# Kernel optimization log

Measured on AMD Instinct MI355X. Metric: run time of the kernel, lower is better.

Reference implementation:

```python
import jax, jax.numpy as jnp
import numpy as np

N_NODES = 50000
N_EDGES = 800000
IN_C, HID_C, OUT_C = 128, 128, 64
N_GRAPHS = 64
NEG_SLOPE = 0.2


def setup_inputs() -> dict:
    key = jax.random.key(0)
    ks = jax.random.split(key, 16)
    x = jax.random.normal(ks[0], (N_NODES, IN_C), dtype=jnp.float32)
    edge_index = jax.random.randint(ks[1], (2, N_EDGES), 0, N_NODES, dtype=jnp.int64)
    batch = jnp.sort(jax.random.randint(ks[2], (N_NODES,), 0, N_GRAPHS, dtype=jnp.int64))
    dims = [(IN_C, HID_C), (HID_C, HID_C), (HID_C, OUT_C)]
    inp = {"x": x, "edge_index": edge_index, "batch": batch}
    for l, (din, dout) in enumerate(dims):
        s = 1.0 / np.sqrt(din)
        inp[f"W{l}"] = jax.random.normal(ks[3 + 4 * l], (din, dout), dtype=jnp.float32) * s
        inp[f"as{l}"] = jax.random.normal(ks[4 + 4 * l], (dout,), dtype=jnp.float32) * 0.1
        inp[f"ad{l}"] = jax.random.normal(ks[5 + 4 * l], (dout,), dtype=jnp.float32) * 0.1
        inp[f"b{l}"] = jnp.zeros((dout,), dtype=jnp.float32)
    return inp


def gat_conv(x, src, dst, W, a_src, a_dst, b, n_nodes):
    # h: [N, dout]
    h = x @ W
    alpha_src = h @ a_src  # [N]
    alpha_dst = h @ a_dst  # [N]
    logits = jax.nn.leaky_relu(alpha_src[src] + alpha_dst[dst], NEG_SLOPE)  # [E]
    # segment softmax over incoming edges of each dst node
    m = jax.ops.segment_max(logits, dst, num_segments=n_nodes)
    e = jnp.exp(logits - m[dst])
    denom = jax.ops.segment_sum(e, dst, num_segments=n_nodes)
    alpha = e / denom[dst]  # [E]
    out = jax.ops.segment_sum(alpha[:, None] * h[src], dst, num_segments=n_nodes)
    return out + b


def reference(x, edge_index, batch, W0, as0, ad0, b0, W1, as1, ad1, b1, W2, as2, ad2, b2):
    n = x.shape[0]
    # add self loops (PyG GATConv default)
    loop = jnp.arange(n, dtype=edge_index.dtype)
    src = jnp.concatenate([edge_index[0], loop])
    dst = jnp.concatenate([edge_index[1], loop])
    h = jax.nn.relu(gat_conv(x, src, dst, W0, as0, ad0, b0, n))
    h = jax.nn.relu(gat_conv(h, src, dst, W1, as1, ad1, b1, n))
    h = gat_conv(h, src, dst, W2, as2, ad2, b2, n)
    # global_add_pool
    return jax.ops.segment_sum(h, batch, num_segments=N_GRAPHS)
```

## Files before the change

### kernel.cpp

```cpp
#include <hip/hip_runtime.h>
#include <hip/hip_fp16.h>
#include <math.h>

#define N_NODES 50000
#define N_EDGES 800000
#define N_GRAPHS 64
#define NEG_SLOPE 0.2f
#define SLOTS 64

#define BIN_NODES 256
#define NBINS 196
#define CAP 6144
#define P1_BLOCKS 192
#define BATCH 2048

typedef _Float16 f16x8 __attribute__((ext_vector_type(8)));
typedef float f32x4 __attribute__((ext_vector_type(4)));

__device__ __forceinline__ float leaky(float x) {
    return x > 0.f ? x : NEG_SLOPE * x;
}

struct __align__(8) half4 {
    __half2 a, b;
};

__global__ __launch_bounds__(256) void prep_kernel(const float* __restrict__ W0,
                                                   const float* __restrict__ W1,
                                                   const float* __restrict__ W2,
                                                   _Float16* __restrict__ Wt0,
                                                   _Float16* __restrict__ Wt1,
                                                   _Float16* __restrict__ Wt2,
                                                   unsigned int* __restrict__ bin_cursor) {
    const int t = blockIdx.x * 256 + threadIdx.x;
    if (t < NBINS) bin_cursor[t] = 0;
    const float* W;
    _Float16* Wt;
    int g, CTl, DOUTl;
    if (t < 2048) { W = W0; Wt = Wt0; g = t; CTl = 8; DOUTl = 128; }
    else if (t < 4096) { W = W1; Wt = Wt1; g = t - 2048; CTl = 8; DOUTl = 128; }
    else if (t < 5120) { W = W2; Wt = Wt2; g = t - 4096; CTl = 4; DOUTl = 64; }
    else return;
    const int kt = g / (CTl * 64);
    const int rem = g % (CTl * 64);
    const int ct = rem / 64;
    const int lane = rem % 64;
    const int kbase = kt * 32 + (lane >> 4) * 8;
    const int c = ct * 16 + (lane & 15);
#pragma unroll
    for (int b = 0; b < 8; ++b)
        Wt[(size_t)g * 8 + b] = (_Float16)W[(size_t)(kbase + b) * DOUTl + c];
}

template <int DOUT>
__device__ __forceinline__ void mfma_gemm_body(const float* __restrict__ X,
                                               const _Float16* __restrict__ Wt,
                                               const float* __restrict__ a_src,
                                               const float* __restrict__ a_dst,
                                               _Float16* __restrict__ H,
                                               float* __restrict__ as_,
                                               float* __restrict__ ad_, int N, int bid,
                                               _Float16* xs) {
    constexpr int CT = DOUT / 16;
    const int tid = threadIdx.x;
    const int n0 = bid * 64;
    const float4* X4 = reinterpret_cast<const float4*>(X);

    for (int idx = tid; idx < 64 * 16; idx += 256) {
        const int r = idx >> 4, q = idx & 15;
        const int n = n0 + r;
        float4 v0 = make_float4(0.f, 0.f, 0.f, 0.f), v1 = v0;
        if (n < N) {
            v0 = X4[(size_t)n * 32 + 2 * q];
            v1 = X4[(size_t)n * 32 + 2 * q + 1];
        }
        f16x8 hv;
        hv[0] = (_Float16)v0.x; hv[1] = (_Float16)v0.y;
        hv[2] = (_Float16)v0.z; hv[3] = (_Float16)v0.w;
        hv[4] = (_Float16)v1.x; hv[5] = (_Float16)v1.y;
        hv[6] = (_Float16)v1.z; hv[7] = (_Float16)v1.w;
        *reinterpret_cast<f16x8*>(&xs[r * 128 + ((q ^ (r & 15)) << 3)]) = hv;
    }
    __syncthreads();

    const int wave = tid >> 6, lane = tid & 63;
    const int colb = lane & 15;
    const int kg = lane >> 4;
    const int arow = wave * 16 + colb;

    f32x4 acc[CT];
#pragma unroll
    for (int ct = 0; ct < CT; ++ct) {
        acc[ct][0] = 0.f; acc[ct][1] = 0.f; acc[ct][2] = 0.f; acc[ct][3] = 0.f;
    }
    const f16x8* Wt8 = reinterpret_cast<const f16x8*>(Wt);
#pragma unroll
    for (int kt = 0; kt < 4; ++kt) {
        f16x8 A = *reinterpret_cast<const f16x8*>(
            &xs[arow * 128 + (((kt * 4 + kg) ^ (arow & 15)) << 3)]);
#pragma unroll
        for (int ct = 0; ct < CT; ++ct) {
            f16x8 B = Wt8[(kt * CT + ct) * 64 + lane];
            acc[ct] = __builtin_amdgcn_mfma_f32_16x16x32_f16(A, B, acc[ct], 0, 0, 0);
        }
    }

    float ps[4] = {0.f, 0.f, 0.f, 0.f}, pd[4] = {0.f, 0.f, 0.f, 0.f};
#pragma unroll
    for (int ct = 0; ct < CT; ++ct) {
        const int col = ct * 16 + colb;
        const float asv = a_src[col];
        const float adv = a_dst[col];
#pragma unroll
        for (int r = 0; r < 4; ++r) {
            const float d = acc[ct][r];
            ps[r] += d * asv;
            pd[r] += d * adv;
            const int row = n0 + wave * 16 + kg * 4 + r;
            if (row < N) H[(size_t)row * DOUT + col] = (_Float16)d;
        }
    }
#pragma unroll
    for (int off = 1; off < 16; off <<= 1) {
#pragma unroll
        for (int r = 0; r < 4; ++r) {
            ps[r] += __shfl_xor(ps[r], off, 64);
            pd[r] += __shfl_xor(pd[r], off, 64);
        }
    }
    if (colb == 0) {
#pragma unroll
        for (int r = 0; r < 4; ++r) {
            const int row = n0 + wave * 16 + kg * 4 + r;
            if (row < N) {
                as_[row] = ps[r];
                ad_[row] = pd[r];
            }
        }
    }
}

template <int DOUT>
__global__ __launch_bounds__(256) void mfma_gemm_kernel(const float* __restrict__ X,
                                                        const _Float16* __restrict__ Wt,
                                                        const float* __restrict__ a_src,
                                                        const float* __restrict__ a_dst,
                                                        _Float16* __restrict__ H,
                                                        float* __restrict__ as_,
                                                        float* __restrict__ ad_, int N) {
    __shared__ __align__(16) _Float16 xs[64 * 128];
    mfma_gemm_body<DOUT>(X, Wt, a_src, a_dst, H, as_, ad_, N, blockIdx.x, xs);
}

struct P1Smem {
    unsigned int stage[BATCH];
    int hist[NBINS];
    int off[NBINS];
    unsigned int gbase[NBINS];
    int total;
};

__device__ __forceinline__ void fill_pass1(const int* __restrict__ src,
                                           const int* __restrict__ dst,
                                           unsigned int* __restrict__ bin_cursor,
                                           unsigned int* __restrict__ bin_buf,
                                           int E, int bid, void* smem_raw) {
    P1Smem& S = *reinterpret_cast<P1Smem*>(smem_raw);
    const int tid = threadIdx.x;
    const int nbatch = (E + BATCH - 1) / BATCH;
    for (int b = bid; b < nbatch; b += P1_BLOCKS) {
        __syncthreads();
        for (int i = tid; i < NBINS; i += 256) S.hist[i] = 0;
        const int e0 = b * BATCH;
        unsigned int pk[8];
        int rk[8];
        bool ok[8];
#pragma unroll
        for (int k = 0; k < 8; ++k) {
            int e = e0 + tid + k * 256;
            ok[k] = (e < E);
            int d = ok[k] ? dst[e] : 0;
            int s = ok[k] ? src[e] : 0;
            pk[k] = ((unsigned)d << 16) | (unsigned)s;
            rk[k] = 0;
        }
        __syncthreads();
#pragma unroll
        for (int k = 0; k < 8; ++k)
            if (ok[k]) rk[k] = atomicAdd(&S.hist[pk[k] >> 24], 1);
        __syncthreads();
        if (tid == 0) {
            int run = 0;
            for (int i = 0; i < NBINS; ++i) {
                S.off[i] = run;
                run += S.hist[i];
            }
            S.total = run;
        }
        __syncthreads();
        if (tid < NBINS && S.hist[tid] > 0)
            S.gbase[tid] = atomicAdd(&bin_cursor[tid], (unsigned)S.hist[tid]);
#pragma unroll
        for (int k = 0; k < 8; ++k)
            if (ok[k]) S.stage[S.off[pk[k] >> 24] + rk[k]] = pk[k];
        __syncthreads();
        const int tot = S.total;
        for (int i = tid; i < tot; i += 256) {
            unsigned int v = S.stage[i];
            int bn = v >> 24;
            unsigned int p = S.gbase[bn] + (unsigned)(i - S.off[bn]);
            if (p < CAP) bin_buf[(size_t)bn * CAP + p] = v;
        }
    }
}

__global__ __launch_bounds__(256) void gemm0_fill_kernel(
    const float* __restrict__ X, const _Float16* __restrict__ Wt0,
    const float* __restrict__ a_src, const float* __restrict__ a_dst,
    _Float16* __restrict__ H, float* __restrict__ as_, float* __restrict__ ad_, int N,
    const int* __restrict__ src, const int* __restrict__ dst,
    unsigned int* __restrict__ bin_cursor, unsigned int* __restrict__ bin_buf, int E) {
    __shared__ __align__(16) unsigned char smem[16384];
    if (blockIdx.x < P1_BLOCKS) {
        fill_pass1(src, dst, bin_cursor, bin_buf, E, blockIdx.x, smem);
        return;
    }
    mfma_gemm_body<128>(X, Wt0, a_src, a_dst, H, as_, ad_, N, blockIdx.x - P1_BLOCKS,
                        reinterpret_cast<_Float16*>(smem));
}

__global__ __launch_bounds__(256) void fill_pass2(const unsigned int* __restrict__ bin_cursor,
                                                  const unsigned int* __restrict__ bin_buf,
                                                  int* __restrict__ cursor,
                                                  unsigned short* __restrict__ col, int N) {
    __shared__ unsigned short bk[BIN_NODES][SLOTS];
    __shared__ int cnt[BIN_NODES];
    const int b = blockIdx.x;
    const int tid = threadIdx.x;
    const int base = b * BIN_NODES;
    const int nn = min(BIN_NODES, N - base);
    if (nn <= 0) return;
    cnt[tid] = 0;
    __syncthreads();
    const int ec = min((int)bin_cursor[b], CAP);
    for (int i = tid; i < ec; i += 256) {
        unsigned int v = bin_buf[(size_t)b * CAP + i];
        int d = (int)(v >> 16) - base;
        int p = atomicAdd(&cnt[d], 1);
        if (p < SLOTS) bk[d][p] = (unsigned short)(v & 0xFFFFu);
    }
    __syncthreads();
    unsigned int* col32 = reinterpret_cast<unsigned int*>(col);
    const unsigned int* lds32 = reinterpret_cast<const unsigned int*>(&bk[0][0]);
    const int words = nn * (SLOTS / 2);
    for (int i = tid; i < words; i += 256)
        col32[(size_t)base * (SLOTS / 2) + i] = lds32[i];
    if (tid < nn) cursor[base + tid] = cnt[tid];
}

template <int DOUT, bool RELU>
__global__ __launch_bounds__(256) void gather_kernel(const half4* __restrict__ H,
                                                     const float* __restrict__ as_,
                                                     const float* __restrict__ ad_,
                                                     const int* __restrict__ cursor,
                                                     const unsigned short* __restrict__ col,
                                                     const float* __restrict__ bias,
                                                     float* __restrict__ OUT, int N) {
    constexpr int NCH4 = DOUT / 4;
    constexpr int SUBS = 64 / NCH4;
    const int node = blockIdx.x * 4 + (threadIdx.x >> 6);
    if (node >= N) return;
    const int l = threadIdx.x & 63;
    const int ch = l & (NCH4 - 1);
    const int sub = l / NCH4;

    const float adn = ad_[node];
    const float sl = leaky(as_[node] + adn);
    const int rs = node << 6;
    const int re = rs + min(cursor[node], SLOTS);

    float4 acc = make_float4(0.f, 0.f, 0.f, 0.f);
    float dsum = 0.f;

    int i = rs + sub;
    for (; i + 7 * SUBS < re; i += 8 * SUBS) {
        int s[8];
        float a[8];
        half4 h[8];
#pragma unroll
        for (int u = 0; u < 8; ++u) s[u] = col[i + u * SUBS];
#pragma unroll
        for (int u = 0; u < 8; ++u) a[u] = as_[s[u]];
#pragma unroll
        for (int u = 0; u < 8; ++u) h[u] = H[(size_t)s[u] * NCH4 + ch];
#pragma unroll
        for (int u = 0; u < 8; ++u) {
            float ee = __expf(leaky(a[u] + adn));
            float2 f0 = __half22float2(h[u].a);
            float2 f1 = __half22float2(h[u].b);
            acc.x += ee * f0.x;
            acc.y += ee * f0.y;
            acc.z += ee * f1.x;
            acc.w += ee * f1.y;
            dsum += ee;
        }
    }
    for (; i + 3 * SUBS < re; i += 4 * SUBS) {
        int s[4];
        float a[4];
        half4 h[4];
#pragma unroll
        for (int u = 0; u < 4; ++u) s[u] = col[i + u * SUBS];
#pragma unroll
        for (int u = 0; u < 4; ++u) a[u] = as_[s[u]];
#pragma unroll
        for (int u = 0; u < 4; ++u) h[u] = H[(size_t)s[u] * NCH4 + ch];
#pragma unroll
        for (int u = 0; u < 4; ++u) {
            float ee = __expf(leaky(a[u] + adn));
            float2 f0 = __half22float2(h[u].a);
            float2 f1 = __half22float2(h[u].b);
            acc.x += ee * f0.x;
            acc.y += ee * f0.y;
            acc.z += ee * f1.x;
            acc.w += ee * f1.y;
            dsum += ee;
        }
    }
    for (; i < re; i += SUBS) {
        int s0 = col[i];
        float e0 = __expf(leaky(as_[s0] + adn));
        half4 h0 = H[(size_t)s0 * NCH4 + ch];
        float2 f0 = __half22float2(h0.a);
        float2 f1 = __half22float2(h0.b);
        acc.x += e0 * f0.x;
        acc.y += e0 * f0.y;
        acc.z += e0 * f1.x;
        acc.w += e0 * f1.y;
        dsum += e0;
    }

#pragma unroll
    for (int off = 32; off >= NCH4; off >>= 1)
        dsum += __shfl_xor(dsum, off, 64);
#pragma unroll
    for (int off = 32; off >= NCH4; off >>= 1) {
        acc.x += __shfl_down(acc.x, off, 64);
        acc.y += __shfl_down(acc.y, off, 64);
        acc.z += __shfl_down(acc.z, off, 64);
        acc.w += __shfl_down(acc.w, off, 64);
    }

    if (l < NCH4) {
        const float e_self = __expf(sl);
        half4 h = H[(size_t)node * NCH4 + ch];
        float2 f0 = __half22float2(h.a);
        float2 f1 = __half22float2(h.b);
        acc.x += e_self * f0.x;
        acc.y += e_self * f0.y;
        acc.z += e_self * f1.x;
        acc.w += e_self * f1.y;
        const float inv = 1.f / (dsum + e_self);
        const float4 b4 = reinterpret_cast<const float4*>(bias)[ch];
        float4 r;
        r.x = acc.x * inv + b4.x;
        r.y = acc.y * inv + b4.y;
        r.z = acc.z * inv + b4.z;
        r.w = acc.w * inv + b4.w;
        if (RELU) {
            r.x = fmaxf(r.x, 0.f);
            r.y = fmaxf(r.y, 0.f);
            r.z = fmaxf(r.z, 0.f);
            r.w = fmaxf(r.w, 0.f);
        }
        reinterpret_cast<float4*>(OUT)[(size_t)node * NCH4 + ch] = r;
    }
}

__global__ __launch_bounds__(256) void pool_kernel(const float* __restrict__ H2,
                                                   const int* __restrict__ batch,
                                                   float* __restrict__ out, int N) {
    const int wv = threadIdx.x >> 6;
    const int c = threadIdx.x & 63;
    const int n0 = blockIdx.x * 128 + wv * 32;
    if (n0 >= N) return;
    const int n1 = min(n0 + 32, N);
    float acc = 0.f;
    int cur = batch[n0];
    for (int n = n0; n < n1; ++n) {
        int g = batch[n];
        if (g != cur) {
            atomicAdd(&out[cur * 64 + c], acc);
            acc = 0.f;
            cur = g;
        }
        acc += H2[n * 64 + c];
    }
    atomicAdd(&out[cur * 64 + c], acc);
}

extern "C" void kernel_launch(void* const* d_in, const int* in_sizes, int n_in,
                              void* d_out, int out_size, void* d_ws, size_t ws_size,
                              hipStream_t stream) {
    const float* x = (const float*)d_in[0];
    const int* edge_index = (const int*)d_in[1];
    const int* batch = (const int*)d_in[2];
    const float* W0 = (const float*)d_in[3];
    const float* as0 = (const float*)d_in[4];
    const float* ad0 = (const float*)d_in[5];
    const float* b0 = (const float*)d_in[6];
    const float* W1 = (const float*)d_in[7];
    const float* as1 = (const float*)d_in[8];
    const float* ad1 = (const float*)d_in[9];
    const float* b1 = (const float*)d_in[10];
    const float* W2 = (const float*)d_in[11];
    const float* as2 = (const float*)d_in[12];
    const float* ad2 = (const float*)d_in[13];
    const float* b2 = (const float*)d_in[14];

    const int* e_src = edge_index;
    const int* e_dst = edge_index + N_EDGES;

    char* p = (char*)d_ws;
    float* B0 = (float*)p;            p += (size_t)N_NODES * 128 * 4;
    _Float16* H = (_Float16*)p;       p += (size_t)N_NODES * 128 * 2;
    float* as_ = (float*)p;           p += (size_t)N_NODES * 4;
    float* ad_ = (float*)p;           p += (size_t)N_NODES * 4;
    int* cursor = (int*)p;            p += (size_t)N_NODES * 4;
    unsigned short* col = (unsigned short*)p; p += (size_t)N_NODES * SLOTS * 2;
    unsigned int* bin_cursor = (unsigned int*)p; p += (size_t)NBINS * 4;
    unsigned int* bin_buf = (unsigned int*)p; p += (size_t)NBINS * CAP * 4;
    _Float16* Wt0 = (_Float16*)p;     p += (size_t)16384 * 2;
    _Float16* Wt1 = (_Float16*)p;     p += (size_t)16384 * 2;
    _Float16* Wt2 = (_Float16*)p;     p += (size_t)8192 * 2;

    const int NODE_BLOCKS = (N_NODES + 3) / 4;
    const int GEMM_BLOCKS = (N_NODES + 63) / 64;

    prep_kernel<<<20, 256, 0, stream>>>(W0, W1, W2, Wt0, Wt1, Wt2, bin_cursor);

    gemm0_fill_kernel<<<P1_BLOCKS + GEMM_BLOCKS, 256, 0, stream>>>(
        x, Wt0, as0, ad0, H, as_, ad_, N_NODES, e_src, e_dst, bin_cursor, bin_buf, N_EDGES);
    fill_pass2<<<NBINS, 256, 0, stream>>>(bin_cursor, bin_buf, cursor, col, N_NODES);
    gather_kernel<128, true><<<NODE_BLOCKS, 256, 0, stream>>>(
        (const half4*)H, as_, ad_, cursor, col, b0, B0, N_NODES);

    mfma_gemm_kernel<128><<<GEMM_BLOCKS, 256, 0, stream>>>(B0, Wt1, as1, ad1, H, as_, ad_, N_NODES);
    gather_kernel<128, true><<<NODE_BLOCKS, 256, 0, stream>>>(
        (const half4*)H, as_, ad_, cursor, col, b1, B0, N_NODES);

    mfma_gemm_kernel<64><<<GEMM_BLOCKS, 256, 0, stream>>>(B0, Wt2, as2, ad2, H, as_, ad_, N_NODES);
    gather_kernel<64, false><<<NODE_BLOCKS, 256, 0, stream>>>(
        (const half4*)H, as_, ad_, cursor, col, b2, B0, N_NODES);

    hipMemsetAsync(d_out, 0, (size_t)out_size * sizeof(float), stream);
    pool_kernel<<<(N_NODES + 127) / 128, 256, 0, stream>>>(B0, batch, (float*)d_out, N_NODES);
}
```

Before: 267.6 us.

## Fuse pooling into last gather, store fp16 activations, widen gather loads

Several changes at once. The intermediate layer outputs are now stored as fp16 rather than fp32, which halves activation write and read traffic, and the GEMM gains an fp16 input path. The gather kernel now loads 8 fp16 channels per lane instead of 4, drops the 8-way unrolled loop, and fuses global add pooling into the final layer with per-block shared-memory reduction. The output zeroing moves into prep_kernel, and the serial single-thread histogram prefix in pass1 becomes a parallel scan. The fp16 intermediates reduce precision, and the fused pool reads batch[node] without bounds guards for node >= N in the last block (N is divisible by 4, so this is safe here).

```diff
diff --git a/kernel.cpp b/kernel.cpp
--- a/kernel.cpp
+++ b/kernel.cpp
@@ -21,8 +21,8 @@
     return x > 0.f ? x : NEG_SLOPE * x;
 }
 
-struct __align__(8) half4 {
-    __half2 a, b;
+struct __align__(16) half8 {
+    __half2 h[4];
 };
 
 __global__ __launch_bounds__(256) void prep_kernel(const float* __restrict__ W0,
@@ -31,9 +31,11 @@
                                                    _Float16* __restrict__ Wt0,
                                                    _Float16* __restrict__ Wt1,
                                                    _Float16* __restrict__ Wt2,
-                                                   unsigned int* __restrict__ bin_cursor) {
+                                                   unsigned int* __restrict__ bin_cursor,
+                                                   float* __restrict__ dout, int osz) {
     const int t = blockIdx.x * 256 + threadIdx.x;
     if (t < NBINS) bin_cursor[t] = 0;
+    if (t < osz) dout[t] = 0.f;
     const float* W;
     _Float16* Wt;
     int g, CTl, DOUTl;
@@ -52,8 +54,8 @@
         Wt[(size_t)g * 8 + b] = (_Float16)W[(size_t)(kbase + b) * DOUTl + c];
 }
 
-template <int DOUT>
-__device__ __forceinline__ void mfma_gemm_body(const float* __restrict__ X,
+template <int DOUT, typename XT>
+__device__ __forceinline__ void mfma_gemm_body(const XT* __restrict__ X,
                                                const _Float16* __restrict__ Wt,
                                                const float* __restrict__ a_src,
                                                const float* __restrict__ a_dst,
@@ -64,22 +66,33 @@
     constexpr int CT = DOUT / 16;
     const int tid = threadIdx.x;
     const int n0 = bid * 64;
-    const float4* X4 = reinterpret_cast<const float4*>(X);
-
-    for (int idx = tid; idx < 64 * 16; idx += 256) {
-        const int r = idx >> 4, q = idx & 15;
-        const int n = n0 + r;
-        float4 v0 = make_float4(0.f, 0.f, 0.f, 0.f), v1 = v0;
-        if (n < N) {
-            v0 = X4[(size_t)n * 32 + 2 * q];
-            v1 = X4[(size_t)n * 32 + 2 * q + 1];
-        }
-        f16x8 hv;
-        hv[0] = (_Float16)v0.x; hv[1] = (_Float16)v0.y;
-        hv[2] = (_Float16)v0.z; hv[3] = (_Float16)v0.w;
-        hv[4] = (_Float16)v1.x; hv[5] = (_Float16)v1.y;
-        hv[6] = (_Float16)v1.z; hv[7] = (_Float16)v1.w;
-        *reinterpret_cast<f16x8*>(&xs[r * 128 + ((q ^ (r & 15)) << 3)]) = hv;
+
+    if constexpr (sizeof(XT) == 4) {
+        const float4* X4 = reinterpret_cast<const float4*>(X);
+        for (int idx = tid; idx < 64 * 16; idx += 256) {
+            const int r = idx >> 4, q = idx & 15;
+            const int n = n0 + r;
+            float4 v0 = make_float4(0.f, 0.f, 0.f, 0.f), v1 = v0;
+            if (n < N) {
+                v0 = X4[(size_t)n * 32 + 2 * q];
+                v1 = X4[(size_t)n * 32 + 2 * q + 1];
+            }
+            f16x8 hv;
+            hv[0] = (_Float16)v0.x; hv[1] = (_Float16)v0.y;
+            hv[2] = (_Float16)v0.z; hv[3] = (_Float16)v0.w;
+            hv[4] = (_Float16)v1.x; hv[5] = (_Float16)v1.y;
+            hv[6] = (_Float16)v1.z; hv[7] = (_Float16)v1.w;
+            *reinterpret_cast<f16x8*>(&xs[r * 128 + ((q ^ (r & 15)) << 3)]) = hv;
+        }
+    } else {
+        const f16x8* X8 = reinterpret_cast<const f16x8*>(X);
+        for (int idx = tid; idx < 64 * 16; idx += 256) {
+            const int r = idx >> 4, q = idx & 15;
+            const int n = n0 + r;
+            f16x8 hv = {};
+            if (n < N) hv = X8[(size_t)n * 16 + q];
+            *reinterpret_cast<f16x8*>(&xs[r * 128 + ((q ^ (r & 15)) << 3)]) = hv;
+        }
     }
     __syncthreads();
 
@@ -140,8 +153,8 @@
     }
 }
 
-template <int DOUT>
-__global__ __launch_bounds__(256) void mfma_gemm_kernel(const float* __restrict__ X,
+template <int DOUT, typename XT>
+__global__ __launch_bounds__(256) void mfma_gemm_kernel(const XT* __restrict__ X,
                                                         const _Float16* __restrict__ Wt,
                                                         const float* __restrict__ a_src,
                                                         const float* __restrict__ a_dst,
@@ -149,7 +162,7 @@
                                                         float* __restrict__ as_,
                                                         float* __restrict__ ad_, int N) {
     __shared__ __align__(16) _Float16 xs[64 * 128];
-    mfma_gemm_body<DOUT>(X, Wt, a_src, a_dst, H, as_, ad_, N, blockIdx.x, xs);
+    mfma_gemm_body<DOUT, XT>(X, Wt, a_src, a_dst, H, as_, ad_, N, blockIdx.x, xs);
 }
 
 struct P1Smem {
@@ -189,14 +202,19 @@
         for (int k = 0; k < 8; ++k)
             if (ok[k]) rk[k] = atomicAdd(&S.hist[pk[k] >> 24], 1);
         __syncthreads();
-        if (tid == 0) {
-            int run = 0;
-            for (int i = 0; i < NBINS; ++i) {
-                S.off[i] = run;
-                run += S.hist[i];
-            }
-            S.total = run;
-        }
+        for (int i = tid; i < NBINS; i += 256) S.off[i] = S.hist[i];
+        __syncthreads();
+#pragma unroll
+        for (int d = 1; d < 256; d <<= 1) {
+            int v = 0;
+            if (tid < NBINS && tid >= d) v = S.off[tid - d];
+            __syncthreads();
+            if (tid < NBINS) S.off[tid] += v;
+            __syncthreads();
+        }
+        if (tid == NBINS - 1) S.total = S.off[NBINS - 1];
+        __syncthreads();
+        if (tid < NBINS) S.off[tid] -= S.hist[tid];
         __syncthreads();
         if (tid < NBINS && S.hist[tid] > 0)
             S.gbase[tid] = atomicAdd(&bin_cursor[tid], (unsigned)S.hist[tid]);
@@ -225,8 +243,8 @@
         fill_pass1(src, dst, bin_cursor, bin_buf, E, blockIdx.x, smem);
         return;
     }
-    mfma_gemm_body<128>(X, Wt0, a_src, a_dst, H, as_, ad_, N, blockIdx.x - P1_BLOCKS,
-                        reinterpret_cast<_Float16*>(smem));
+    mfma_gemm_body<128, float>(X, Wt0, a_src, a_dst, H, as_, ad_, N, blockIdx.x - P1_BLOCKS,
+                               reinterpret_cast<_Float16*>(smem));
 }
 
 __global__ __launch_bounds__(256) void fill_pass2(const unsigned int* __restrict__ bin_cursor,
@@ -258,145 +276,144 @@
     if (tid < nn) cursor[base + tid] = cnt[tid];
 }
 
-template <int DOUT, bool RELU>
-__global__ __launch_bounds__(256) void gather_kernel(const half4* __restrict__ H,
+template <int DOUT, bool POOL>
+__global__ __launch_bounds__(256) void gather_kernel(const half8* __restrict__ H8,
                                                      const float* __restrict__ as_,
                                                      const float* __restrict__ ad_,
                                                      const int* __restrict__ cursor,
                                                      const unsigned short* __restrict__ col,
                                                      const float* __restrict__ bias,
-                                                     float* __restrict__ OUT, int N) {
-    constexpr int NCH4 = DOUT / 4;
-    constexpr int SUBS = 64 / NCH4;
-    const int node = blockIdx.x * 4 + (threadIdx.x >> 6);
-    if (node >= N) return;
+                                                     half8* __restrict__ OUT,
+                                                     const int* __restrict__ batch,
+                                                     float* __restrict__ pool_out, int N) {
+    constexpr int NCH = DOUT / 8;
+    constexpr int SUBS = 64 / NCH;
+    __shared__ float pbuf[4][64];
+    __shared__ int pg[4];
+    const int wv = threadIdx.x >> 6;
+    const int node = blockIdx.x * 4 + wv;
+    if (!POOL && node >= N) return;
     const int l = threadIdx.x & 63;
-    const int ch = l & (NCH4 - 1);
-    const int sub = l / NCH4;
+    const int ch = l & (NCH - 1);
+    const int sub = l / NCH;
 
     const float adn = ad_[node];
     const float sl = leaky(as_[node] + adn);
     const int rs = node << 6;
     const int re = rs + min(cursor[node], SLOTS);
 
-    float4 acc = make_float4(0.f, 0.f, 0.f, 0.f);
+    float acc[8] = {};
     float dsum = 0.f;
 
     int i = rs + sub;
-    for (; i + 7 * SUBS < re; i += 8 * SUBS) {
-        int s[8];
-        float a[8];
-        half4 h[8];
-#pragma unroll
-        for (int u = 0; u < 8; ++u) s[u] = col[i + u * SUBS];
-#pragma unroll
-        for (int u = 0; u < 8; ++u) a[u] = as_[s[u]];
-#pragma unroll
-        for (int u = 0; u < 8; ++u) h[u] = H[(size_t)s[u] * NCH4 + ch];
-#pragma unroll
-        for (int u = 0; u < 8; ++u) {
-            float ee = __expf(leaky(a[u] + adn));
-            float2 f0 = __half22float2(h[u].a);
-            float2 f1 = __half22float2(h[u].b);
-            acc.x += ee * f0.x;
-            acc.y += ee * f0.y;
-            acc.z += ee * f1.x;
-            acc.w += ee * f1.y;
-            dsum += ee;
-        }
-    }
     for (; i + 3 * SUBS < re; i += 4 * SUBS) {
         int s[4];
         float a[4];
-        half4 h[4];
+        half8 h[4];
 #pragma unroll
         for (int u = 0; u < 4; ++u) s[u] = col[i + u * SUBS];
 #pragma unroll
         for (int u = 0; u < 4; ++u) a[u] = as_[s[u]];
 #pragma unroll
-        for (int u = 0; u < 4; ++u) h[u] = H[(size_t)s[u] * NCH4 + ch];
+        for (int u = 0; u < 4; ++u) h[u] = H8[(size_t)s[u] * NCH + ch];
 #pragma unroll
         for (int u = 0; u < 4; ++u) {
             float ee = __expf(leaky(a[u] + adn));
-            float2 f0 = __half22float2(h[u].a);
-            float2 f1 = __half22float2(h[u].b);
-            acc.x += ee * f0.x;
-            acc.y += ee * f0.y;
-            acc.z += ee * f1.x;
-            acc.w += ee * f1.y;
+#pragma unroll
+            for (int j = 0; j < 4; ++j) {
+                float2 f = __half22float2(h[u].h[j]);
+                acc[2 * j] += ee * f.x;
+                acc[2 * j + 1] += ee * f.y;
+            }
             dsum += ee;
         }
     }
-    for (; i < re; i += SUBS) {
+    for (; i + SUBS < re; i += 2 * SUBS) {
+        int s0 = col[i], s1 = col[i + SUBS];
+        float a0 = as_[s0], a1 = as_[s1];
+        half8 h0 = H8[(size_t)s0 * NCH + ch];
+        half8 h1 = H8[(size_t)s1 * NCH + ch];
+        float e0 = __expf(leaky(a0 + adn));
+        float e1 = __expf(leaky(a1 + adn));
+#pragma unroll
+        for (int j = 0; j < 4; ++j) {
+            float2 f0 = __half22float2(h0.h[j]);
+            float2 f1 = __half22float2(h1.h[j]);
+            acc[2 * j] += e0 * f0.x + e1 * f1.x;
+            acc[2 * j + 1] += e0 * f0.y + e1 * f1.y;
+        }
+        dsum += e0 + e1;
+    }
+    if (i < re) {
         int s0 = col[i];
         float e0 = __expf(leaky(as_[s0] + adn));
-        half4 h0 = H[(size_t)s0 * NCH4 + ch];
-        float2 f0 = __half22float2(h0.a);
-        float2 f1 = __half22float2(h0.b);
-        acc.x += e0 * f0.x;
-        acc.y += e0 * f0.y;
-        acc.z += e0 * f1.x;
-        acc.w += e0 * f1.y;
+        half8 h0 = H8[(size_t)s0 * NCH + ch];
+#pragma unroll
+        for (int j = 0; j < 4; ++j) {
+            float2 f = __half22float2(h0.h[j]);
+            acc[2 * j] += e0 * f.x;
+            acc[2 * j + 1] += e0 * f.y;
+        }
         dsum += e0;
     }
 
 #pragma unroll
-    for (int off = 32; off >= NCH4; off >>= 1)
+    for (int off = 32; off >= NCH; off >>= 1)
         dsum += __shfl_xor(dsum, off, 64);
 #pragma unroll
-    for (int off = 32; off >= NCH4; off >>= 1) {
-        acc.x += __shfl_down(acc.x, off, 64);
-        acc.y += __shfl_down(acc.y, off, 64);
-        acc.z += __shfl_down(acc.z, off, 64);
-        acc.w += __shfl_down(acc.w, off, 64);
-    }
-
-    if (l < NCH4) {
+    for (int off = 32; off >= NCH; off >>= 1) {
+#pragma unroll
+        for (int j = 0; j < 8; ++j)
+            acc[j] += __shfl_down(acc[j], off, 64);
+    }
+
+    if (l < NCH) {
         const float e_self = __expf(sl);
-        half4 h = H[(size_t)node * NCH4 + ch];
-        float2 f0 = __half22float2(h.a);
-        float2 f1 = __half22float2(h.b);
-        acc.x += e_self * f0.x;
-        acc.y += e_self * f0.y;
-        acc.z += e_self * f1.x;
-        acc.w += e_self * f1.y;
-        const float inv = 1.f / (dsum + e_self);
-        const float4 b4 = reinterpret_cast<const float4*>(bias)[ch];
-        float4 r;
-        r.x = acc.x * inv + b4.x;
-        r.y = acc.y * inv + b4.y;
-        r.z = acc.z * inv + b4.z;
-        r.w = acc.w * inv + b4.w;
-        if (RELU) {
-            r.x = fmaxf(r.x, 0.f);
-            r.y = fmaxf(r.y, 0.f);
-            r.z = fmaxf(r.z, 0.f);
-            r.w = fmaxf(r.w, 0.f);
-        }
-        reinterpret_cast<float4*>(OUT)[(size_t)node * NCH4 + ch] = r;
-    }
-}
-
-__global__ __launch_bounds__(256) void pool_kernel(const float* __restrict__ H2,
-                                                   const int* __restrict__ batch,
-                                                   float* __restrict__ out, int N) {
-    const int wv = threadIdx.x >> 6;
-    const int c = threadIdx.x & 63;
-    const int n0 = blockIdx.x * 128 + wv * 32;
-    if (n0 >= N) return;
-    const int n1 = min(n0 + 32, N);
-    float acc = 0.f;
-    int cur = batch[n0];
-    for (int n = n0; n < n1; ++n) {
-        int g = batch[n];
-        if (g != cur) {
-            atomicAdd(&out[cur * 64 + c], acc);
-            acc = 0.f;
-            cur = g;
-        }
-        acc += H2[n * 64 + c];
-    }
-    atomicAdd(&out[cur * 64 + c], acc);
+        half8 h = H8[(size_t)node * NCH + ch];
+        const float inv_pre = dsum + e_self;
+        const float inv = 1.f / inv_pre;
+        const float4* b4 = reinterpret_cast<const float4*>(bias);
+        const float4 ba = b4[2 * ch], bb = b4[2 * ch + 1];
+        const float bj[8] = {ba.x, ba.y, ba.z, ba.w, bb.x, bb.y, bb.z, bb.w};
+        float r[8];
+#pragma unroll
+        for (int j = 0; j < 4; ++j) {
+            float2 f = __half22float2(h.h[j]);
+            acc[2 * j] += e_self * f.x;
+            acc[2 * j + 1] += e_self * f.y;
+        }
+#pragma unroll
+        for (int j = 0; j < 8; ++j) {
+            r[j] = acc[j] * inv + bj[j];
+            if (!POOL) r[j] = fmaxf(r[j], 0.f);
+        }
+        if (POOL) {
+#pragma unroll
+            for (int j = 0; j < 8; ++j) pbuf[wv][ch * 8 + j] = r[j];
+        } else {
+            half8 o;
+#pragma unroll
+            for (int j = 0; j < 4; ++j)
+                o.h[j] = __floats2half2_rn(r[2 * j], r[2 * j + 1]);
+            OUT[(size_t)node * NCH + ch] = o;
+        }
+    }
+    if (POOL) {
+        if (l == 0) pg[wv] = batch[node];
+        __syncthreads();
+        if (threadIdx.x < 64) {
+            const int c = threadIdx.x;
+            const int g0 = pg[0], g3 = pg[3];
+            if (g0 == g3) {
+                atomicAdd(&pool_out[g0 * 64 + c],
+                          pbuf[0][c] + pbuf[1][c] + pbuf[2][c] + pbuf[3][c]);
+            } else {
+#pragma unroll
+                for (int w = 0; w < 4; ++w)
+                    atomicAdd(&pool_out[pg[w] * 64 + c], pbuf[w][c]);
+            }
+        }
+    }
 }
 
 extern "C" void kernel_launch(void* const* d_in, const int* in_sizes, int n_in,
@@ -422,13 +439,13 @@
     const int* e_dst = edge_index + N_EDGES;
 
     char* p = (char*)d_ws;
-    float* B0 = (float*)p;            p += (size_t)N_NODES * 128 * 4;
+    _Float16* X16 = (_Float16*)p;     p += (size_t)N_NODES * 128 * 2;
     _Float16* H = (_Float16*)p;       p += (size_t)N_NODES * 128 * 2;
     float* as_ = (float*)p;           p += (size_t)N_NODES * 4;
     float* ad_ = (float*)p;           p += (size_t)N_NODES * 4;
     int* cursor = (int*)p;            p += (size_t)N_NODES * 4;
     unsigned short* col = (unsigned short*)p; p += (size_t)N_NODES * SLOTS * 2;
-    unsigned int* bin_cursor = (unsigned int*)p; p += (size_t)NBINS * 4;
+    unsigned int* bin_cursor = (unsigned int*)p; p += (size_t)((NBINS + 3) & ~3) * 4;
     unsigned int* bin_buf = (unsigned int*)p; p += (size_t)NBINS * CAP * 4;
     _Float16* Wt0 = (_Float16*)p;     p += (size_t)16384 * 2;
     _Float16* Wt1 = (_Float16*)p;     p += (size_t)16384 * 2;
@@ -437,22 +454,22 @@
     const int NODE_BLOCKS = (N_NODES + 3) / 4;
     const int GEMM_BLOCKS = (N_NODES + 63) / 64;
 
-    prep_kernel<<<20, 256, 0, stream>>>(W0, W1, W2, Wt0, Wt1, Wt2, bin_cursor);
+    prep_kernel<<<20, 256, 0, stream>>>(W0, W1, W2, Wt0, Wt1, Wt2, bin_cursor,
+                                        (float*)d_out, out_size);
 
     gemm0_fill_kernel<<<P1_BLOCKS + GEMM_BLOCKS, 256, 0, stream>>>(
         x, Wt0, as0, ad0, H, as_, ad_, N_NODES, e_src, e_dst, bin_cursor, bin_buf, N_EDGES);
     fill_pass2<<<NBINS, 256, 0, stream>>>(bin_cursor, bin_buf, cursor, col, N_NODES);
-    gather_kernel<128, true><<<NODE_BLOCKS, 256, 0, stream>>>(
-        (const half4*)H, as_, ad_, cursor, col, b0, B0, N_NODES);
-
-    mfma_gemm_kernel<128><<<GEMM_BLOCKS, 256, 0, stream>>>(B0, Wt1, as1, ad1, H, as_, ad_, N_NODES);
-    gather_kernel<128, true><<<NODE_BLOCKS, 256, 0, stream>>>(
-        (const half4*)H, as_, ad_, cursor, col, b1, B0, N_NODES);
-
-    mfma_gemm_kernel<64><<<GEMM_BLOCKS, 256, 0, stream>>>(B0, Wt2, as2, ad2, H, as_, ad_, N_NODES);
-    gather_kernel<64, false><<<NODE_BLOCKS, 256, 0, stream>>>(
-        (const half4*)H, as_, ad_, cursor, col, b2, B0, N_NODES);
-
-    hipMemsetAsync(d_out, 0, (size_t)out_size * sizeof(float), stream);
-    pool_kernel<<<(N_NODES + 127) / 128, 256, 0, stream>>>(B0, batch, (float*)d_out, N_NODES);
-}
+    gather_kernel<128, false><<<NODE_BLOCKS, 256, 0, stream>>>(
+        (const half8*)H, as_, ad_, cursor, col, b0, (half8*)X16, batch, nullptr, N_NODES);
+
+    mfma_gemm_kernel<128, _Float16><<<GEMM_BLOCKS, 256, 0, stream>>>(
+        X16, Wt1, as1, ad1, H, as_, ad_, N_NODES);
+    gather_kernel<128, false><<<NODE_BLOCKS, 256, 0, stream>>>(
+        (const half8*)H, as_, ad_, cursor, col, b1, (half8*)X16, batch, nullptr, N_NODES);
+
+    mfma_gemm_kernel<64, _Float16><<<GEMM_BLOCKS, 256, 0, stream>>>(
+        X16, Wt2, as2, ad2, H, as_, ad_, N_NODES);
+    gather_kernel<64, true><<<NODE_BLOCKS, 256, 0, stream>>>(
+        (const half8*)H, as_, ad_, cursor, col, b2, nullptr, batch, (float*)d_out, N_NODES);
+}
```

New measurement: 250.8 us (median of 2 runs). -6.3%, faster.
